# Optimization experiments

Measured on AMD Instinct MI355X. Metric: run time of the kernel, lower is better.

Reference implementation:

```python
import jax, jax.numpy as jnp
import numpy as np

N_NODES = 100000

def setup_inputs() -> dict:
    key = jax.random.key(0)
    k1, k2, k3, k4 = jax.random.split(key, 4)
    B, S, D, H = 50000, 10, 128, 128
    nodes = jax.random.randint(k1, (B,), 0, N_NODES, dtype=jnp.int64 if jax.config.jax_enable_x64 else jnp.int32)
    neigh_idx = jax.random.randint(k2, (B, S), 0, N_NODES, dtype=nodes.dtype)
    feature = jax.random.normal(k3, (N_NODES, D), dtype=jnp.float32)
    weight = jax.random.normal(k4, (2 * D, H), dtype=jnp.float32) * (1.0 / np.sqrt(2 * D))
    return {"nodes": nodes, "neigh_idx": neigh_idx, "feature": feature, "weight": weight}

def reference(nodes, neigh_idx, feature, weight):
    # Mean aggregation over sampled neighbors: [B, S, D] -> [B, D]
    neigh_feats = jnp.mean(feature[neigh_idx], axis=1)
    # Self features: [B, D]
    self_feats = feature[nodes]
    # Concat + linear + ReLU (gcn=False branch)
    combined = jnp.concatenate([self_feats, neigh_feats], axis=1)  # [B, 2D]
    return jax.nn.relu(combined @ weight)  # [B, H]
```

## Files before the change

### kernel.cpp

```cpp
#include <hip/hip_runtime.h>


typedef __attribute__((ext_vector_type(8))) short bf16x8;
typedef __attribute__((ext_vector_type(4))) float f32x4;

__device__ __forceinline__ unsigned short f2bf(float x) {
  unsigned int u = __float_as_uint(x);
  u += 0x7fffu + ((u >> 16) & 1u);
  return (unsigned short)(u >> 16);
}

__global__ void sage_prep_wt(const float* __restrict__ W,
                             unsigned short* __restrict__ Wt) {
  int tid = blockIdx.x * blockDim.x + threadIdx.x;
  float4 v = ((const float4*)W)[tid];
  int flat = tid << 2;
  int k = flat >> 7;
  int h = flat & 127;
  Wt[(h + 0) * 256 + k] = f2bf(v.x);
  Wt[(h + 1) * 256 + k] = f2bf(v.y);
  Wt[(h + 2) * 256 + k] = f2bf(v.z);
  Wt[(h + 3) * 256 + k] = f2bf(v.w);
}

__global__ __launch_bounds__(512, 6)
void sage_fused4(const int* __restrict__ nodes,
                 const int* __restrict__ neigh,
                 const float* __restrict__ feat,
                 const unsigned short* __restrict__ Wt,
                 float* __restrict__ out, int B)
{
  constexpr int K = 256, H = 128, S = 10;
  constexpr int TILE = 32;
  constexpr int STR = K + 8;
  __shared__ unsigned short Clds[TILE * STR];

  const int t = threadIdx.x;
  const int block0 = blockIdx.x * TILE;

  {
    const int rh  = t >> 5;
    const int sub = t & 31;
    const float4* f4 = (const float4*)feat;

#pragma unroll
    for (int half = 0; half < 2; ++half) {
      const int r = rh + half * 16;
      const int b = block0 + r;
      unsigned short* crow = &Clds[r * STR];
      if (b < B) {
        const long srow = (long)nodes[b] * 32;
        float4 sv = f4[srow + sub];

        float ax = 0.f, ay = 0.f, az = 0.f, aw = 0.f;
#pragma unroll
        for (int s = 0; s < S; ++s) {
          const long nrow = (long)neigh[b * S + s] * 32;
          float4 v = f4[nrow + sub];
          ax += v.x; ay += v.y; az += v.z; aw += v.w;
        }
        ushort4 o;
        o.x = f2bf(sv.x); o.y = f2bf(sv.y); o.z = f2bf(sv.z); o.w = f2bf(sv.w);
        *(ushort4*)&crow[4 * sub] = o;
        o.x = f2bf(ax * 0.1f); o.y = f2bf(ay * 0.1f);
        o.z = f2bf(az * 0.1f); o.w = f2bf(aw * 0.1f);
        *(ushort4*)&crow[128 + 4 * sub] = o;
      } else {
        ushort4 z; z.x = z.y = z.z = z.w = 0;
        *(ushort4*)&crow[4 * sub] = z;
        *(ushort4*)&crow[128 + 4 * sub] = z;
      }
    }
  }
  __syncthreads();
  __builtin_amdgcn_sched_barrier(0);

  const int lane = t & 63;
  const int wave = t >> 6;
  const int m    = lane & 15;
  const int quad = lane >> 4;
  const int cbase = wave * 16;

  bf16x8 bfrag[8];
#pragma unroll
  for (int ks = 0; ks < 8; ++ks)
    bfrag[ks] = *(const bf16x8*)&Wt[(cbase + m) * K + ks * 32 + quad * 8];

  f32x4 acc0 = {0.f, 0.f, 0.f, 0.f};
  f32x4 acc1 = {0.f, 0.f, 0.f, 0.f};
#pragma unroll
  for (int ks = 0; ks < 8; ++ks) {
    const int koff = ks * 32 + quad * 8;
    bf16x8 a0 = *(const bf16x8*)&Clds[(m     ) * STR + koff];
    bf16x8 a1 = *(const bf16x8*)&Clds[(16 + m) * STR + koff];
    acc0 = __builtin_amdgcn_mfma_f32_16x16x32_bf16(a0, bfrag[ks], acc0, 0, 0, 0);
    acc1 = __builtin_amdgcn_mfma_f32_16x16x32_bf16(a1, bfrag[ks], acc1, 0, 0, 0);
  }

#pragma unroll
  for (int reg = 0; reg < 4; ++reg) {
    const int row0 = quad * 4 + reg;
    const int gb0 = block0 + row0;
    const int gb1 = gb0 + 16;
    if (gb0 < B) out[(size_t)gb0 * H + cbase + m] = fmaxf(acc0[reg], 0.0f);
    if (gb1 < B) out[(size_t)gb1 * H + cbase + m] = fmaxf(acc1[reg], 0.0f);
  }
}

extern "C" void kernel_launch(void* const* d_in, const int* in_sizes, int n_in,
                              void* d_out, int out_size, void* d_ws, size_t ws_size,
                              hipStream_t stream) {
  const int*   nodes = (const int*)d_in[0];
  const int*   neigh = (const int*)d_in[1];
  const float* feat  = (const float*)d_in[2];
  const float* W     = (const float*)d_in[3];
  float*       out   = (float*)d_out;
  const int B = in_sizes[0];

  unsigned short* Wt = (unsigned short*)d_ws;
  sage_prep_wt<<<32, 256, 0, stream>>>(W, Wt);
  const int grid = (B + 31) / 32;
  sage_fused4<<<grid, 512, 0, stream>>>(nodes, neigh, feat, Wt, out, B);
}
```

Baseline: 130.7 us.

## Double row tile to 64 per block and transpose weights via LDS tile

The fused gather+GEMM kernel now handles 64 rows per block instead of 32. The per-wave B fragments loaded from the transposed weights are reused across four MFMA row groups, which halves weight reloads per row and the number of blocks. The launch-bounds occupancy hint drops from 6 to 4 and LDS per block doubles, which may reduce how many waves are in flight to hide gather latency. The weight transpose prep kernel now stages through shared memory so its global writes are coalesced.

```diff
diff --git a/kernel.cpp b/kernel.cpp
--- a/kernel.cpp
+++ b/kernel.cpp
@@ -10,28 +10,46 @@
   return (unsigned short)(u >> 16);
 }
 
-__global__ void sage_prep_wt(const float* __restrict__ W,
-                             unsigned short* __restrict__ Wt) {
-  int tid = blockIdx.x * blockDim.x + threadIdx.x;
-  float4 v = ((const float4*)W)[tid];
-  int flat = tid << 2;
-  int k = flat >> 7;
-  int h = flat & 127;
-  Wt[(h + 0) * 256 + k] = f2bf(v.x);
-  Wt[(h + 1) * 256 + k] = f2bf(v.y);
-  Wt[(h + 2) * 256 + k] = f2bf(v.z);
-  Wt[(h + 3) * 256 + k] = f2bf(v.w);
+__global__ void sage_prep_wt2(const float* __restrict__ W,
+                              unsigned short* __restrict__ Wt) {
+  __shared__ float tile[32][132];
+  const int t = threadIdx.x;
+  const int kbase = blockIdx.x * 32;
+  const float4* w4 = (const float4*)(W + (size_t)kbase * 128);
+#pragma unroll
+  for (int j = 0; j < 4; ++j) {
+    int f4i = t + j * 256;
+    float4 v = w4[f4i];
+    int flat = f4i << 2;
+    int kk = flat >> 7;
+    int h  = flat & 127;
+    tile[kk][h] = v.x; tile[kk][h + 1] = v.y;
+    tile[kk][h + 2] = v.z; tile[kk][h + 3] = v.w;
+  }
+  __syncthreads();
+  const int h  = t >> 1;
+  const int kc = (t & 1) * 16;
+  unsigned short* dst = &Wt[(size_t)h * 256 + kbase + kc];
+#pragma unroll
+  for (int j = 0; j < 4; ++j) {
+    ushort4 o;
+    o.x = f2bf(tile[kc + 4 * j + 0][h]);
+    o.y = f2bf(tile[kc + 4 * j + 1][h]);
+    o.z = f2bf(tile[kc + 4 * j + 2][h]);
+    o.w = f2bf(tile[kc + 4 * j + 3][h]);
+    *(ushort4*)&dst[4 * j] = o;
+  }
 }
 
-__global__ __launch_bounds__(512, 6)
-void sage_fused4(const int* __restrict__ nodes,
+__global__ __launch_bounds__(512, 4)
+void sage_fused6(const int* __restrict__ nodes,
                  const int* __restrict__ neigh,
                  const float* __restrict__ feat,
                  const unsigned short* __restrict__ Wt,
                  float* __restrict__ out, int B)
 {
   constexpr int K = 256, H = 128, S = 10;
-  constexpr int TILE = 32;
+  constexpr int TILE = 64;
   constexpr int STR = K + 8;
   __shared__ unsigned short Clds[TILE * STR];
 
@@ -39,15 +57,15 @@
   const int block0 = blockIdx.x * TILE;
 
   {
-    const int rh  = t >> 5;
+    const int r   = t >> 5;
     const int sub = t & 31;
     const float4* f4 = (const float4*)feat;
 
 #pragma unroll
-    for (int half = 0; half < 2; ++half) {
-      const int r = rh + half * 16;
-      const int b = block0 + r;
-      unsigned short* crow = &Clds[r * STR];
+    for (int half = 0; half < 4; ++half) {
+      const int row = r + half * 16;
+      const int b = block0 + row;
+      unsigned short* crow = &Clds[row * STR];
       if (b < B) {
         const long srow = (long)nodes[b] * 32;
         float4 sv = f4[srow + sub];
@@ -88,13 +106,19 @@
 
   f32x4 acc0 = {0.f, 0.f, 0.f, 0.f};
   f32x4 acc1 = {0.f, 0.f, 0.f, 0.f};
+  f32x4 acc2 = {0.f, 0.f, 0.f, 0.f};
+  f32x4 acc3 = {0.f, 0.f, 0.f, 0.f};
 #pragma unroll
   for (int ks = 0; ks < 8; ++ks) {
     const int koff = ks * 32 + quad * 8;
     bf16x8 a0 = *(const bf16x8*)&Clds[(m     ) * STR + koff];
     bf16x8 a1 = *(const bf16x8*)&Clds[(16 + m) * STR + koff];
+    bf16x8 a2 = *(const bf16x8*)&Clds[(32 + m) * STR + koff];
+    bf16x8 a3 = *(const bf16x8*)&Clds[(48 + m) * STR + koff];
     acc0 = __builtin_amdgcn_mfma_f32_16x16x32_bf16(a0, bfrag[ks], acc0, 0, 0, 0);
     acc1 = __builtin_amdgcn_mfma_f32_16x16x32_bf16(a1, bfrag[ks], acc1, 0, 0, 0);
+    acc2 = __builtin_amdgcn_mfma_f32_16x16x32_bf16(a2, bfrag[ks], acc2, 0, 0, 0);
+    acc3 = __builtin_amdgcn_mfma_f32_16x16x32_bf16(a3, bfrag[ks], acc3, 0, 0, 0);
   }
 
 #pragma unroll
@@ -102,8 +126,12 @@
     const int row0 = quad * 4 + reg;
     const int gb0 = block0 + row0;
     const int gb1 = gb0 + 16;
+    const int gb2 = gb0 + 32;
+    const int gb3 = gb0 + 48;
     if (gb0 < B) out[(size_t)gb0 * H + cbase + m] = fmaxf(acc0[reg], 0.0f);
     if (gb1 < B) out[(size_t)gb1 * H + cbase + m] = fmaxf(acc1[reg], 0.0f);
+    if (gb2 < B) out[(size_t)gb2 * H + cbase + m] = fmaxf(acc2[reg], 0.0f);
+    if (gb3 < B) out[(size_t)gb3 * H + cbase + m] = fmaxf(acc3[reg], 0.0f);
   }
 }
 
@@ -118,7 +146,7 @@
   const int B = in_sizes[0];
 
   unsigned short* Wt = (unsigned short*)d_ws;
-  sage_prep_wt<<<32, 256, 0, stream>>>(W, Wt);
-  const int grid = (B + 31) / 32;
-  sage_fused4<<<grid, 512, 0, stream>>>(nodes, neigh, feat, Wt, out, B);
+  sage_prep_wt2<<<8, 256, 0, stream>>>(W, Wt);
+  const int grid = (B + 63) / 64;
+  sage_fused6<<<grid, 512, 0, stream>>>(nodes, neigh, feat, Wt, out, B);
 }
```

Result: no change. 132.5 us (+1.4%).
